# Optimization experiments

Hardware: AMD Instinct MI355X
Metric: run time of the kernel (lower is better)

The kernel has to match this reference:

```python
import jax, jax.numpy as jnp
import numpy as np

N_NODES = 50000
N_EDGES = 800000
N_ATOMS = 100
HID = 128
N_LAYERS = 3
OUT_LAYERS = 2
OUT_DIM = 1
N_GRAPHS = 1024
EPS = 1e-12  # F.normalize eps


def setup_inputs() -> dict:
    key = jax.random.key(0)
    ks = jax.random.split(key, 12)
    s = 0.05
    x_ori = jax.random.randint(ks[0], (N_NODES,), 0, N_ATOMS)
    edge_index = jax.random.randint(ks[1], (2, N_EDGES), 0, N_NODES)
    edge_attr = jax.random.normal(ks[2], (N_EDGES, 1), jnp.float32)
    batch_ids = jnp.sort(jax.random.randint(ks[3], (N_NODES,), 0, N_GRAPHS))
    embd_w = jax.random.normal(ks[4], (N_ATOMS, HID), jnp.float32) * s
    gamma_w = jnp.ones((N_LAYERS, N_ATOMS, 1), jnp.float32)  # reset_parameters sets ones
    w_atom_W = jax.random.normal(ks[5], (N_LAYERS, HID, HID), jnp.float32) * s
    w_atom_b = jax.random.normal(ks[6], (N_LAYERS, HID), jnp.float32) * s
    lin_W = jax.random.normal(ks[7], (OUT_LAYERS, HID, HID), jnp.float32) * s
    lin_b = jax.random.normal(ks[8], (OUT_LAYERS, HID), jnp.float32) * s
    wp_W = jax.random.normal(ks[9], (HID, OUT_DIM), jnp.float32) * s
    wp_b = jax.random.normal(ks[10], (OUT_DIM,), jnp.float32) * s
    return dict(x_ori=x_ori, edge_index=edge_index, edge_attr=edge_attr,
                batch_ids=batch_ids, embd_w=embd_w, gamma_w=gamma_w,
                w_atom_W=w_atom_W, w_atom_b=w_atom_b, lin_W=lin_W, lin_b=lin_b,
                wp_W=wp_W, wp_b=wp_b)


def reference(x_ori, edge_index, edge_attr, batch_ids, embd_w, gamma_w,
              w_atom_W, w_atom_b, lin_W, lin_b, wp_W, wp_b):
    src, dst = edge_index[0], edge_index[1]
    x = embd_w[x_ori]  # [N, H]
    for l in range(N_LAYERS):
        h = jax.nn.relu(x @ w_atom_W[l] + w_atom_b[l])            # [N, H]
        gam = jax.nn.sigmoid(gamma_w[l])[x_ori][dst]              # [E, 1]
        ew = jnp.exp(-gam * edge_attr ** 2)                       # [E, 1]
        msg = ew * h[src]                                         # [E, H] gather+weight
        agg = jax.ops.segment_sum(msg, dst, num_segments=N_NODES) # scatter-add
        y = agg + x
        nrm = jnp.maximum(jnp.linalg.norm(y, axis=1, keepdims=True), EPS)
        x = y / nrm                                               # F.normalize(., 2, 1)
    for i in range(OUT_LAYERS):
        x = jax.nn.relu(x @ lin_W[i] + lin_b[i])
    m_x = jax.ops.segment_sum(x, batch_ids, num_segments=N_GRAPHS)  # [G, H]
    props = m_x @ wp_W + wp_b                                      # [G, 1]
    return jnp.squeeze(props, axis=1)                              # [G]
```

## Files before the change

### kernel.cpp

```cpp
#include <hip/hip_runtime.h>
#include <hip/hip_bf16.h>
#include <math.h>

typedef __hip_bfloat16 bf16;
typedef unsigned int uint;
typedef unsigned short ushort;
typedef __attribute__((ext_vector_type(8))) short short8;
typedef __attribute__((ext_vector_type(4))) float f32x4;

#define HID 128
#define NN 50000
#define NE 800000
#define NG 1024
#define NA 100
#define CAP 64

__device__ __forceinline__ uint bf16_rne_hi(float f) {
    uint u = __float_as_uint(f);
    return (u + 0x7fffu + ((u >> 16) & 1u)) & 0xffff0000u;
}
__device__ __forceinline__ uint pack_bf16x2(float lo, float hi) {
    return (bf16_rne_hi(lo) >> 16) | bf16_rne_hi(hi);
}
__device__ __forceinline__ ushort bf16_rne(float f) {
    uint u = __float_as_uint(f);
    return (ushort)((u + 0x7fffu + ((u >> 16) & 1u)) >> 16);
}
__device__ __forceinline__ float load_f(const void* p, int i, int f32) {
    return f32 ? ((const float*)p)[i]
               : __uint_as_float((uint)((const ushort*)p)[i] << 16);
}
__device__ __forceinline__ int detect_f32(const void* emb) {
    const ushort* p = (const ushort*)emb;
    int lane = threadIdx.x & 63;
    float v = __uint_as_float((uint)p[lane * 4] << 16);
    int bad0 = (!(v == v) || fabsf(v) > 1e4f || (v != 0.0f && fabsf(v) < 1e-10f));
    float w = __uint_as_float((uint)p[lane * 4 + 2] << 16);
    int bad1 = (!(w == w) || fabsf(w) > 1e4f || (w != 0.0f && fabsf(w) < 1e-10f));
    int cnt = __popcll(__ballot(bad0)) + __popcll(__ballot(bad1));
    return cnt > 16;
}

#define EMB_BLKS   ((NN * 64) / 256)
#define PACKW_BLKS (5 * 16384 / 256)
#define CVT_CNT    (300 + 384 + 256 + 128 + 1)
#define CVT_BLKS   5
#define INITC_BLKS ((NN + 255) / 256)
#define PREP_B1    EMB_BLKS
#define PREP_B2    (PREP_B1 + PACKW_BLKS)
#define PREP_B3    (PREP_B2 + CVT_BLKS)
#define PREP_B4    (PREP_B3 + INITC_BLKS)
#define PREP_B5    (PREP_B4 + 4)
#define PREP_GRID  (PREP_B5 + 1)

__global__ void prep_k(const int* __restrict__ xo, const void* __restrict__ emb,
                       const void* __restrict__ gamw, const void* __restrict__ wAW,
                       const void* __restrict__ wAb, const void* __restrict__ linW,
                       const void* __restrict__ linb, const void* __restrict__ wpW,
                       const void* __restrict__ wpb,
                       uint* __restrict__ xb, ushort* __restrict__ Wp,
                       float* __restrict__ f_sgam, float* __restrict__ f_wAb,
                       float* __restrict__ f_linb, float* __restrict__ f_wp,
                       float* __restrict__ f_wpb, int* __restrict__ cursor,
                       float* __restrict__ grf, int* __restrict__ flag) {
    int f32 = detect_f32(emb);
    int b = blockIdx.x, t = threadIdx.x;
    if (b < PREP_B1) {
        int g = b * 256 + t;
        int node = g >> 6, c2 = g & 63;
        int base = xo[node] * HID + c2 * 2;
        xb[g] = pack_bf16x2(load_f(emb, base, f32), load_f(emb, base + 1, f32));
    } else if (b < PREP_B2) {
        int t2 = (b - PREP_B1) * 256 + t;
        int i   = t2 & 7;
        int n   = (t2 >> 3) & 15;
        int q   = (t2 >> 7) & 3;
        int j16 = (t2 >> 9) & 7;
        int ks  = (t2 >> 12) & 3;
        int mat = t2 >> 14;
        int k = ks * 32 + q * 8 + i;
        int j = j16 * 16 + n;
        const void* W = (mat < 3) ? wAW : linW;
        int off = ((mat < 3) ? mat : (mat - 3)) * 16384 + k * HID + j;
        Wp[t2] = bf16_rne(load_f(W, off, f32));
    } else if (b < PREP_B3) {
        int idx = (b - PREP_B2) * 256 + t;
        if (idx < 300) {
            float v = load_f(gamw, idx, f32);
            f_sgam[idx] = 1.0f / (1.0f + __expf(-v));
        } else if (idx < 684) {
            f_wAb[idx - 300] = load_f(wAb, idx - 300, f32);
        } else if (idx < 940) {
            f_linb[idx - 684] = load_f(linb, idx - 684, f32);
        } else if (idx < 1068) {
            f_wp[idx - 940] = load_f(wpW, idx - 940, f32);
        } else if (idx < CVT_CNT) {
            f_wpb[0] = load_f(wpb, 0, f32);
        }
    } else if (b < PREP_B4) {
        int n = (b - PREP_B3) * 256 + t;
        if (n < NN) cursor[n] = n * CAP;
    } else if (b < PREP_B5) {
        grf[(b - PREP_B4) * 256 + t] = 0.0f;
    } else {
        if (t == 0) *flag = f32;
    }
}

__device__ __forceinline__ void gemm_core(const uint* __restrict__ xb,
                                          const ushort* __restrict__ Wp,
                                          const float* __restrict__ bias,
                                          int m0, int lane,
                                          f32x4 acc0[8], f32x4 acc1[8]) {
    int ln15 = lane & 15;
    int q    = lane >> 4;
    int mA = min(m0 + ln15, NN - 1);
    int mB = min(m0 + 16 + ln15, NN - 1);
    const short8* A8 = (const short8*)xb;
    const short8* B8 = (const short8*)Wp;
#pragma unroll
    for (int j16 = 0; j16 < 8; ++j16) {
        float bv = bias[j16 * 16 + ln15];
        acc0[j16] = (f32x4){bv, bv, bv, bv};
        acc1[j16] = acc0[j16];
    }
#pragma unroll
    for (int ks = 0; ks < 4; ++ks) {
        short8 a0 = A8[mA * 16 + ks * 4 + q];
        short8 a1 = A8[mB * 16 + ks * 4 + q];
#pragma unroll
        for (int j16 = 0; j16 < 8; ++j16) {
            short8 b = B8[(ks * 8 + j16) * 64 + q * 16 + ln15];
            acc0[j16] = __builtin_amdgcn_mfma_f32_16x16x32_bf16(a0, b, acc0[j16], 0, 0, 0);
            acc1[j16] = __builtin_amdgcn_mfma_f32_16x16x32_bf16(a1, b, acc1[j16], 0, 0, 0);
        }
    }
}

__device__ __forceinline__ void gemm_store(f32x4 acc0[8], f32x4 acc1[8],
                                           int m0, int lane, uint* __restrict__ outb) {
    int ln15 = lane & 15;
    int q    = lane >> 4;
    ushort* ob = (ushort*)outb;
#pragma unroll
    for (int reg = 0; reg < 4; ++reg) {
        int n0 = m0 + q * 4 + reg;
        int n1 = n0 + 16;
#pragma unroll
        for (int j16 = 0; j16 < 8; ++j16) {
            if (n0 < NN)
                ob[(size_t)n0 * HID + j16 * 16 + ln15] = bf16_rne(fmaxf(acc0[j16][reg], 0.0f));
            if (n1 < NN)
                ob[(size_t)n1 * HID + j16 * 16 + ln15] = bf16_rne(fmaxf(acc1[j16][reg], 0.0f));
        }
    }
}

#define GEMM_BLKS ((NN + 127) / 128)
#define SCAT_BLKS (NE / 4 / 256)
__global__ __launch_bounds__(256) void work2_k(const uint* __restrict__ xb,
                                               const ushort* __restrict__ Wp,
                                               const float* __restrict__ bias,
                                               uint* __restrict__ outb,
                                               const int* __restrict__ esrc,
                                               const int* __restrict__ edst,
                                               const void* __restrict__ ea,
                                               const void* __restrict__ emb,
                                               int* __restrict__ cursor,
                                               uint* __restrict__ csr) {
    int b = blockIdx.x;
    if (b < GEMM_BLKS) {
        f32x4 acc0[8], acc1[8];
        int m0 = b * 128 + (threadIdx.x >> 6) * 32;
        gemm_core(xb, Wp, bias, m0, threadIdx.x & 63, acc0, acc1);
        gemm_store(acc0, acc1, m0, threadIdx.x & 63, outb);
    } else {
        int f32 = detect_f32(emb);
        int e0 = ((b - GEMM_BLKS) * 256 + threadIdx.x) * 4;
        int4 s4 = *(const int4*)(esrc + e0);
        int4 d4 = *(const int4*)(edst + e0);
        float a0, a1, a2, a3;
        if (f32) {
            float4 f = *(const float4*)((const float*)ea + e0);
            a0 = f.x; a1 = f.y; a2 = f.z; a3 = f.w;
        } else {
            ushort4 u = *(const ushort4*)((const ushort*)ea + e0);
            a0 = __uint_as_float((uint)u.x << 16);
            a1 = __uint_as_float((uint)u.y << 16);
            a2 = __uint_as_float((uint)u.z << 16);
            a3 = __uint_as_float((uint)u.w << 16);
        }
        int p0 = atomicAdd(&cursor[d4.x], 1);
        int p1 = atomicAdd(&cursor[d4.y], 1);
        int p2 = atomicAdd(&cursor[d4.z], 1);
        int p3 = atomicAdd(&cursor[d4.w], 1);
        if (p0 < d4.x * CAP + CAP) csr[p0] = (uint)(s4.x & 0xffff) | bf16_rne_hi(a0 * a0);
        if (p1 < d4.y * CAP + CAP) csr[p1] = (uint)(s4.y & 0xffff) | bf16_rne_hi(a1 * a1);
        if (p2 < d4.z * CAP + CAP) csr[p2] = (uint)(s4.z & 0xffff) | bf16_rne_hi(a2 * a2);
        if (p3 < d4.w * CAP + CAP) csr[p3] = (uint)(s4.w & 0xffff) | bf16_rne_hi(a3 * a3);
    }
}

__global__ __launch_bounds__(512) void gg_k(const int* __restrict__ cursor,
                                            const uint* __restrict__ csr,
                                            const int* __restrict__ xo,
                                            const float* __restrict__ sgam,
                                            const uint* __restrict__ hb_in,
                                            uint* __restrict__ xb,
                                            const ushort* __restrict__ Wp,
                                            const float* __restrict__ bias,
                                            uint* __restrict__ hb_out) {
    __shared__ uint lds_a[2048];
    int t = threadIdx.x;
    int w = t >> 6, lane = t & 63;
    int n0 = blockIdx.x * 32;

#pragma unroll
    for (int j4 = 0; j4 < 4; ++j4) {
        int j = w * 4 + j4;
        int n = n0 + j;
        if (n < NN) {
            int deg = min(cursor[n] - n * CAP, CAP);
            const uint* cp = csr + n * CAP;
            float g = sgam[xo[n]];
            float ax = 0.0f, ay = 0.0f;
            for (int e = 0; e < deg; e += 8) {
                uint4 c0 = *(const uint4*)(cp + e);
                uint4 c1 = *(const uint4*)(cp + e + 4);
                uint cc[8];
                cc[0] = c0.x; cc[1] = c0.y; cc[2] = c0.z; cc[3] = c0.w;
                cc[4] = c1.x; cc[5] = c1.y; cc[6] = c1.z; cc[7] = c1.w;
#pragma unroll
                for (int i = 1; i < 8; ++i) cc[i] = (e + i < deg) ? cc[i] : cc[0];
                uint v[8];
#pragma unroll
                for (int i = 0; i < 8; ++i) v[i] = hb_in[(cc[i] & 0xffffu) * 64 + lane];
                float we[8];
#pragma unroll
                for (int i = 0; i < 8; ++i) {
                    float x = __expf(-g * __uint_as_float(cc[i] & 0xffff0000u));
                    we[i] = (e + i < deg) ? x : 0.0f;
                }
#pragma unroll
                for (int i = 0; i < 8; ++i) {
                    ax = fmaf(we[i], __uint_as_float(v[i] << 16), ax);
                    ay = fmaf(we[i], __uint_as_float(v[i] & 0xffff0000u), ay);
                }
            }
            uint xv = xb[n * 64 + lane];
            float yx = ax + __uint_as_float(xv << 16);
            float yy = ay + __uint_as_float(xv & 0xffff0000u);
            float ss = yx * yx + yy * yy;
#pragma unroll
            for (int m = 32; m; m >>= 1) ss += __shfl_xor(ss, m);
            float inv = 1.0f / fmaxf(sqrtf(ss), 1e-12f);
            uint o = pack_bf16x2(yx * inv, yy * inv);
            xb[n * 64 + lane] = o;
            int rt = j >> 4, m = j & 15;
            int ks = lane >> 4, q = (lane >> 2) & 3;
            lds_a[(((rt * 4 + ks) * 64) + q * 16 + m) * 4 + (lane & 3)] = o;
        }
    }
    __syncthreads();

    int ln15 = lane & 15, q = lane >> 4;
    const short8* A8 = (const short8*)lds_a;
    const short8* B8 = (const short8*)Wp;
    f32x4 acc[2];
    {
        float bv = bias[w * 16 + ln15];
        acc[0] = (f32x4){bv, bv, bv, bv};
        acc[1] = acc[0];
    }
#pragma unroll
    for (int ks = 0; ks < 4; ++ks) {
        short8 b = B8[(ks * 8 + w) * 64 + q * 16 + ln15];
#pragma unroll
        for (int rt = 0; rt < 2; ++rt) {
            short8 a = A8[(rt * 4 + ks) * 64 + lane];
            acc[rt] = __builtin_amdgcn_mfma_f32_16x16x32_bf16(a, b, acc[rt], 0, 0, 0);
        }
    }
    ushort* ob = (ushort*)hb_out;
#pragma unroll
    for (int rt = 0; rt < 2; ++rt) {
#pragma unroll
        for (int reg = 0; reg < 4; ++reg) {
            int n = n0 + rt * 16 + q * 4 + reg;
            if (n < NN)
                ob[(size_t)n * HID + w * 16 + ln15] = bf16_rne(fmaxf(acc[rt][reg], 0.0f));
        }
    }
}

__global__ __launch_bounds__(256) void gemm5_graph_k(const uint* __restrict__ xb,
                                                     const ushort* __restrict__ Wp,
                                                     const float* __restrict__ bias,
                                                     const float* __restrict__ wp,
                                                     const int* __restrict__ batch,
                                                     float* __restrict__ grf) {
    int lane = threadIdx.x & 63;
    int ln15 = lane & 15;
    int q    = lane >> 4;
    int m0 = blockIdx.x * 128 + (threadIdx.x >> 6) * 32;
    f32x4 acc0[8], acc1[8];
    gemm_core(xb, Wp, bias, m0, lane, acc0, acc1);
    float wpv[8];
#pragma unroll
    for (int j16 = 0; j16 < 8; ++j16) wpv[j16] = wp[j16 * 16 + ln15];
#pragma unroll
    for (int half = 0; half < 2; ++half) {
#pragma unroll
        for (int reg = 0; reg < 4; ++reg) {
            float s = 0.0f;
#pragma unroll
            for (int j16 = 0; j16 < 8; ++j16) {
                float v = half ? acc1[j16][reg] : acc0[j16][reg];
                s = fmaf(fmaxf(v, 0.0f), wpv[j16], s);
            }
#pragma unroll
            for (int m = 1; m < 16; m <<= 1) s += __shfl_xor(s, m);
            int n = m0 + half * 16 + q * 4 + reg;
            if (ln15 == 0 && n < NN) atomicAdd(&grf[batch[n]], s);
        }
    }
}

__global__ void out_k(const float* __restrict__ grf, const float* __restrict__ wpb,
                      void* __restrict__ out, const int* __restrict__ flag) {
    int g = blockIdx.x * 256 + threadIdx.x;
    if (g >= NG) return;
    float r = grf[g] + wpb[0];
    if (*flag) ((float*)out)[g] = r;
    else       ((bf16*)out)[g] = __float2bfloat16(r);
}

extern "C" void kernel_launch(void* const* d_in, const int* in_sizes, int n_in,
                              void* d_out, int out_size, void* d_ws, size_t ws_size,
                              hipStream_t stream) {
    const int*  xo    = (const int*)d_in[0];
    const int*  ei    = (const int*)d_in[1];
    const int*  src   = ei;
    const int*  dst   = ei + NE;
    const void* ea    = d_in[2];
    const int*  batch = (const int*)d_in[3];
    const void* emb   = d_in[4];
    const void* gamw  = d_in[5];
    const void* wAW   = d_in[6];
    const void* wAb   = d_in[7];
    const void* linW  = d_in[8];
    const void* linb  = d_in[9];
    const void* wpW   = d_in[10];
    const void* wpb   = d_in[11];

    uint*  xb     = (uint*)d_ws;
    uint*  hA     = xb + (size_t)NN * 64;
    uint*  hB     = hA + (size_t)NN * 64;
    uint*  csr    = hB + (size_t)NN * 64;
    int*   cursor = (int*)(csr + (size_t)NN * CAP);
    float* grf    = (float*)(cursor + NN);
    float* P      = grf + NG;
    float* f_sgam = P;
    float* f_wAb  = f_sgam + 304;
    float* f_linb = f_wAb + 384;
    float* f_wp   = f_linb + 256;
    float* f_wpb  = f_wp + 128;
    int*   flag   = (int*)(f_wpb + 8);
    ushort* Wp    = (ushort*)(flag + 8);

    prep_k<<<PREP_GRID, 256, 0, stream>>>(xo, emb, gamw, wAW, wAb, linW, linb, wpW, wpb,
                                          xb, Wp, f_sgam, f_wAb, f_linb, f_wp, f_wpb,
                                          cursor, grf, flag);

    work2_k<<<GEMM_BLKS + SCAT_BLKS, 256, 0, stream>>>(xb, Wp, f_wAb, hA,
                                                       src, dst, ea, emb, cursor, csr);

    const int GG_GRID = (NN + 31) / 32;
    gg_k<<<GG_GRID, 512, 0, stream>>>(cursor, csr, xo, f_sgam,       hA, xb,
                                      Wp + 1 * 16384, f_wAb + 128, hB);
    gg_k<<<GG_GRID, 512, 0, stream>>>(cursor, csr, xo, f_sgam + 100, hB, xb,
                                      Wp + 2 * 16384, f_wAb + 256, hA);
    gg_k<<<GG_GRID, 512, 0, stream>>>(cursor, csr, xo, f_sgam + 200, hA, xb,
                                      Wp + 3 * 16384, f_linb,       hB);

    gemm5_graph_k<<<GEMM_BLKS, 256, 0, stream>>>(hB, Wp + 4 * 16384, f_linb + HID,
                                                 f_wp, batch, grf);
    out_k<<<(NG + 255) / 256, 256, 0, stream>>>(grf, f_wpb, d_out, flag);
}
```

Baseline: 296.5 us.

## Fuse final MLP layer and graph pooling into last gather layer; restructure prep

```diff
diff --git a/kernel.cpp b/kernel.cpp
--- a/kernel.cpp
+++ b/kernel.cpp
@@ -41,142 +41,33 @@
     return cnt > 16;
 }
 
+#define SCAT_BLKS  (NE / 4 / 256)
 #define EMB_BLKS   ((NN * 64) / 256)
 #define PACKW_BLKS (5 * 16384 / 256)
 #define CVT_CNT    (300 + 384 + 256 + 128 + 1)
 #define CVT_BLKS   5
-#define INITC_BLKS ((NN + 255) / 256)
-#define PREP_B1    EMB_BLKS
-#define PREP_B2    (PREP_B1 + PACKW_BLKS)
-#define PREP_B3    (PREP_B2 + CVT_BLKS)
-#define PREP_B4    (PREP_B3 + INITC_BLKS)
-#define PREP_B5    (PREP_B4 + 4)
-#define PREP_GRID  (PREP_B5 + 1)
-
-__global__ void prep_k(const int* __restrict__ xo, const void* __restrict__ emb,
-                       const void* __restrict__ gamw, const void* __restrict__ wAW,
-                       const void* __restrict__ wAb, const void* __restrict__ linW,
-                       const void* __restrict__ linb, const void* __restrict__ wpW,
-                       const void* __restrict__ wpb,
-                       uint* __restrict__ xb, ushort* __restrict__ Wp,
-                       float* __restrict__ f_sgam, float* __restrict__ f_wAb,
-                       float* __restrict__ f_linb, float* __restrict__ f_wp,
-                       float* __restrict__ f_wpb, int* __restrict__ cursor,
-                       float* __restrict__ grf, int* __restrict__ flag) {
+#define W1_B1      SCAT_BLKS
+#define W1_B2      (W1_B1 + EMB_BLKS)
+#define W1_B3      (W1_B2 + PACKW_BLKS)
+#define W1_B4      (W1_B3 + CVT_BLKS)
+#define W1_GRID    (W1_B4 + 1)
+
+__global__ void work1_k(const int* __restrict__ xo, const void* __restrict__ emb,
+                        const void* __restrict__ gamw, const void* __restrict__ wAW,
+                        const void* __restrict__ wAb, const void* __restrict__ linW,
+                        const void* __restrict__ linb, const void* __restrict__ wpW,
+                        const void* __restrict__ wpb,
+                        const int* __restrict__ esrc, const int* __restrict__ edst,
+                        const void* __restrict__ ea,
+                        uint* __restrict__ xb, ushort* __restrict__ Wp,
+                        float* __restrict__ f_sgam, float* __restrict__ f_wAb,
+                        float* __restrict__ f_linb, float* __restrict__ f_wp,
+                        float* __restrict__ f_wpb, int* __restrict__ cursor,
+                        uint* __restrict__ csr, int* __restrict__ flag) {
     int f32 = detect_f32(emb);
     int b = blockIdx.x, t = threadIdx.x;
-    if (b < PREP_B1) {
-        int g = b * 256 + t;
-        int node = g >> 6, c2 = g & 63;
-        int base = xo[node] * HID + c2 * 2;
-        xb[g] = pack_bf16x2(load_f(emb, base, f32), load_f(emb, base + 1, f32));
-    } else if (b < PREP_B2) {
-        int t2 = (b - PREP_B1) * 256 + t;
-        int i   = t2 & 7;
-        int n   = (t2 >> 3) & 15;
-        int q   = (t2 >> 7) & 3;
-        int j16 = (t2 >> 9) & 7;
-        int ks  = (t2 >> 12) & 3;
-        int mat = t2 >> 14;
-        int k = ks * 32 + q * 8 + i;
-        int j = j16 * 16 + n;
-        const void* W = (mat < 3) ? wAW : linW;
-        int off = ((mat < 3) ? mat : (mat - 3)) * 16384 + k * HID + j;
-        Wp[t2] = bf16_rne(load_f(W, off, f32));
-    } else if (b < PREP_B3) {
-        int idx = (b - PREP_B2) * 256 + t;
-        if (idx < 300) {
-            float v = load_f(gamw, idx, f32);
-            f_sgam[idx] = 1.0f / (1.0f + __expf(-v));
-        } else if (idx < 684) {
-            f_wAb[idx - 300] = load_f(wAb, idx - 300, f32);
-        } else if (idx < 940) {
-            f_linb[idx - 684] = load_f(linb, idx - 684, f32);
-        } else if (idx < 1068) {
-            f_wp[idx - 940] = load_f(wpW, idx - 940, f32);
-        } else if (idx < CVT_CNT) {
-            f_wpb[0] = load_f(wpb, 0, f32);
-        }
-    } else if (b < PREP_B4) {
-        int n = (b - PREP_B3) * 256 + t;
-        if (n < NN) cursor[n] = n * CAP;
-    } else if (b < PREP_B5) {
-        grf[(b - PREP_B4) * 256 + t] = 0.0f;
-    } else {
-        if (t == 0) *flag = f32;
-    }
-}
-
-__device__ __forceinline__ void gemm_core(const uint* __restrict__ xb,
-                                          const ushort* __restrict__ Wp,
-                                          const float* __restrict__ bias,
-                                          int m0, int lane,
-                                          f32x4 acc0[8], f32x4 acc1[8]) {
-    int ln15 = lane & 15;
-    int q    = lane >> 4;
-    int mA = min(m0 + ln15, NN - 1);
-    int mB = min(m0 + 16 + ln15, NN - 1);
-    const short8* A8 = (const short8*)xb;
-    const short8* B8 = (const short8*)Wp;
-#pragma unroll
-    for (int j16 = 0; j16 < 8; ++j16) {
-        float bv = bias[j16 * 16 + ln15];
-        acc0[j16] = (f32x4){bv, bv, bv, bv};
-        acc1[j16] = acc0[j16];
-    }
-#pragma unroll
-    for (int ks = 0; ks < 4; ++ks) {
-        short8 a0 = A8[mA * 16 + ks * 4 + q];
-        short8 a1 = A8[mB * 16 + ks * 4 + q];
-#pragma unroll
-        for (int j16 = 0; j16 < 8; ++j16) {
-            short8 b = B8[(ks * 8 + j16) * 64 + q * 16 + ln15];
-            acc0[j16] = __builtin_amdgcn_mfma_f32_16x16x32_bf16(a0, b, acc0[j16], 0, 0, 0);
-            acc1[j16] = __builtin_amdgcn_mfma_f32_16x16x32_bf16(a1, b, acc1[j16], 0, 0, 0);
-        }
-    }
-}
-
-__device__ __forceinline__ void gemm_store(f32x4 acc0[8], f32x4 acc1[8],
-                                           int m0, int lane, uint* __restrict__ outb) {
-    int ln15 = lane & 15;
-    int q    = lane >> 4;
-    ushort* ob = (ushort*)outb;
-#pragma unroll
-    for (int reg = 0; reg < 4; ++reg) {
-        int n0 = m0 + q * 4 + reg;
-        int n1 = n0 + 16;
-#pragma unroll
-        for (int j16 = 0; j16 < 8; ++j16) {
-            if (n0 < NN)
-                ob[(size_t)n0 * HID + j16 * 16 + ln15] = bf16_rne(fmaxf(acc0[j16][reg], 0.0f));
-            if (n1 < NN)
-                ob[(size_t)n1 * HID + j16 * 16 + ln15] = bf16_rne(fmaxf(acc1[j16][reg], 0.0f));
-        }
-    }
-}
-
-#define GEMM_BLKS ((NN + 127) / 128)
-#define SCAT_BLKS (NE / 4 / 256)
-__global__ __launch_bounds__(256) void work2_k(const uint* __restrict__ xb,
-                                               const ushort* __restrict__ Wp,
-                                               const float* __restrict__ bias,
-                                               uint* __restrict__ outb,
-                                               const int* __restrict__ esrc,
-                                               const int* __restrict__ edst,
-                                               const void* __restrict__ ea,
-                                               const void* __restrict__ emb,
-                                               int* __restrict__ cursor,
-                                               uint* __restrict__ csr) {
-    int b = blockIdx.x;
-    if (b < GEMM_BLKS) {
-        f32x4 acc0[8], acc1[8];
-        int m0 = b * 128 + (threadIdx.x >> 6) * 32;
-        gemm_core(xb, Wp, bias, m0, threadIdx.x & 63, acc0, acc1);
-        gemm_store(acc0, acc1, m0, threadIdx.x & 63, outb);
-    } else {
-        int f32 = detect_f32(emb);
-        int e0 = ((b - GEMM_BLKS) * 256 + threadIdx.x) * 4;
+    if (b < W1_B1) {
+        int e0 = (b * 256 + t) * 4;
         int4 s4 = *(const int4*)(esrc + e0);
         int4 d4 = *(const int4*)(edst + e0);
         float a0, a1, a2, a3;
@@ -194,13 +85,103 @@
         int p1 = atomicAdd(&cursor[d4.y], 1);
         int p2 = atomicAdd(&cursor[d4.z], 1);
         int p3 = atomicAdd(&cursor[d4.w], 1);
-        if (p0 < d4.x * CAP + CAP) csr[p0] = (uint)(s4.x & 0xffff) | bf16_rne_hi(a0 * a0);
-        if (p1 < d4.y * CAP + CAP) csr[p1] = (uint)(s4.y & 0xffff) | bf16_rne_hi(a1 * a1);
-        if (p2 < d4.z * CAP + CAP) csr[p2] = (uint)(s4.z & 0xffff) | bf16_rne_hi(a2 * a2);
-        if (p3 < d4.w * CAP + CAP) csr[p3] = (uint)(s4.w & 0xffff) | bf16_rne_hi(a3 * a3);
-    }
-}
-
+        if (p0 < CAP) csr[d4.x * CAP + p0] = (uint)(s4.x & 0xffff) | bf16_rne_hi(a0 * a0);
+        if (p1 < CAP) csr[d4.y * CAP + p1] = (uint)(s4.y & 0xffff) | bf16_rne_hi(a1 * a1);
+        if (p2 < CAP) csr[d4.z * CAP + p2] = (uint)(s4.z & 0xffff) | bf16_rne_hi(a2 * a2);
+        if (p3 < CAP) csr[d4.w * CAP + p3] = (uint)(s4.w & 0xffff) | bf16_rne_hi(a3 * a3);
+    } else if (b < W1_B2) {
+        int g = (b - W1_B1) * 256 + t;
+        int node = g >> 6, c2 = g & 63;
+        int base = xo[node] * HID + c2 * 2;
+        xb[g] = pack_bf16x2(load_f(emb, base, f32), load_f(emb, base + 1, f32));
+    } else if (b < W1_B3) {
+        int t2 = (b - W1_B2) * 256 + t;
+        int i   = t2 & 7;
+        int n   = (t2 >> 3) & 15;
+        int q   = (t2 >> 7) & 3;
+        int j16 = (t2 >> 9) & 7;
+        int ks  = (t2 >> 12) & 3;
+        int mat = t2 >> 14;
+        int k = ks * 32 + q * 8 + i;
+        int j = j16 * 16 + n;
+        const void* W = (mat < 3) ? wAW : linW;
+        int off = ((mat < 3) ? mat : (mat - 3)) * 16384 + k * HID + j;
+        Wp[t2] = bf16_rne(load_f(W, off, f32));
+    } else if (b < W1_B4) {
+        int idx = (b - W1_B3) * 256 + t;
+        if (idx < 300) {
+            float v = load_f(gamw, idx, f32);
+            f_sgam[idx] = 1.0f / (1.0f + __expf(-v));
+        } else if (idx < 684) {
+            f_wAb[idx - 300] = load_f(wAb, idx - 300, f32);
+        } else if (idx < 940) {
+            f_linb[idx - 684] = load_f(linb, idx - 684, f32);
+        } else if (idx < 1068) {
+            f_wp[idx - 940] = load_f(wpW, idx - 940, f32);
+        } else if (idx < CVT_CNT) {
+            f_wpb[0] = load_f(wpb, 0, f32);
+        }
+    } else {
+        if (t == 0) *flag = f32;
+    }
+}
+
+__device__ __forceinline__ void gemm_core(const uint* __restrict__ xb,
+                                          const ushort* __restrict__ Wp,
+                                          const float* __restrict__ bias,
+                                          int m0, int lane,
+                                          f32x4 acc0[8], f32x4 acc1[8]) {
+    int ln15 = lane & 15;
+    int q    = lane >> 4;
+    int mA = min(m0 + ln15, NN - 1);
+    int mB = min(m0 + 16 + ln15, NN - 1);
+    const short8* A8 = (const short8*)xb;
+    const short8* B8 = (const short8*)Wp;
+#pragma unroll
+    for (int j16 = 0; j16 < 8; ++j16) {
+        float bv = bias[j16 * 16 + ln15];
+        acc0[j16] = (f32x4){bv, bv, bv, bv};
+        acc1[j16] = acc0[j16];
+    }
+#pragma unroll
+    for (int ks = 0; ks < 4; ++ks) {
+        short8 a0 = A8[mA * 16 + ks * 4 + q];
+        short8 a1 = A8[mB * 16 + ks * 4 + q];
+#pragma unroll
+        for (int j16 = 0; j16 < 8; ++j16) {
+            short8 b = B8[(ks * 8 + j16) * 64 + q * 16 + ln15];
+            acc0[j16] = __builtin_amdgcn_mfma_f32_16x16x32_bf16(a0, b, acc0[j16], 0, 0, 0);
+            acc1[j16] = __builtin_amdgcn_mfma_f32_16x16x32_bf16(a1, b, acc1[j16], 0, 0, 0);
+        }
+    }
+}
+
+#define GEMM_BLKS ((NN + 127) / 128)
+__global__ __launch_bounds__(256) void gemm_mfma_k(const uint* __restrict__ xb,
+                                                   const ushort* __restrict__ Wp,
+                                                   const float* __restrict__ bias,
+                                                   uint* __restrict__ outb) {
+    int lane = threadIdx.x & 63;
+    int ln15 = lane & 15, q = lane >> 4;
+    int m0 = blockIdx.x * 128 + (threadIdx.x >> 6) * 32;
+    f32x4 acc0[8], acc1[8];
+    gemm_core(xb, Wp, bias, m0, lane, acc0, acc1);
+    ushort* ob = (ushort*)outb;
+#pragma unroll
+    for (int reg = 0; reg < 4; ++reg) {
+        int n0 = m0 + q * 4 + reg;
+        int n1 = n0 + 16;
+#pragma unroll
+        for (int j16 = 0; j16 < 8; ++j16) {
+            if (n0 < NN)
+                ob[(size_t)n0 * HID + j16 * 16 + ln15] = bf16_rne(fmaxf(acc0[j16][reg], 0.0f));
+            if (n1 < NN)
+                ob[(size_t)n1 * HID + j16 * 16 + ln15] = bf16_rne(fmaxf(acc1[j16][reg], 0.0f));
+        }
+    }
+}
+
+template <int LAST>
 __global__ __launch_bounds__(512) void gg_k(const int* __restrict__ cursor,
                                             const uint* __restrict__ csr,
                                             const int* __restrict__ xo,
@@ -209,8 +190,15 @@
                                             uint* __restrict__ xb,
                                             const ushort* __restrict__ Wp,
                                             const float* __restrict__ bias,
-                                            uint* __restrict__ hb_out) {
+                                            uint* __restrict__ hb_out,
+                                            const ushort* __restrict__ Wp2,
+                                            const float* __restrict__ bias2,
+                                            const float* __restrict__ wp,
+                                            const int* __restrict__ batch,
+                                            float* __restrict__ grf) {
     __shared__ uint lds_a[2048];
+    __shared__ ushort lds_h[LAST ? 16384 / 2 : 2];
+    __shared__ float lds_g[LAST ? 32 : 1];
     int t = threadIdx.x;
     int w = t >> 6, lane = t & 63;
     int n0 = blockIdx.x * 32;
@@ -220,7 +208,7 @@
         int j = w * 4 + j4;
         int n = n0 + j;
         if (n < NN) {
-            int deg = min(cursor[n] - n * CAP, CAP);
+            int deg = min(cursor[n], CAP);
             const uint* cp = csr + n * CAP;
             float g = sgam[xo[n]];
             float ax = 0.0f, ay = 0.0f;
@@ -255,12 +243,13 @@
             for (int m = 32; m; m >>= 1) ss += __shfl_xor(ss, m);
             float inv = 1.0f / fmaxf(sqrtf(ss), 1e-12f);
             uint o = pack_bf16x2(yx * inv, yy * inv);
-            xb[n * 64 + lane] = o;
+            if (!LAST) xb[n * 64 + lane] = o;
             int rt = j >> 4, m = j & 15;
             int ks = lane >> 4, q = (lane >> 2) & 3;
             lds_a[(((rt * 4 + ks) * 64) + q * 16 + m) * 4 + (lane & 3)] = o;
         }
     }
+    if (LAST && t < 32) lds_g[t] = 0.0f;
     __syncthreads();
 
     int ln15 = lane & 15, q = lane >> 4;
@@ -281,48 +270,67 @@
             acc[rt] = __builtin_amdgcn_mfma_f32_16x16x32_bf16(a, b, acc[rt], 0, 0, 0);
         }
     }
-    ushort* ob = (ushort*)hb_out;
+    if (!LAST) {
+        ushort* ob = (ushort*)hb_out;
+#pragma unroll
+        for (int rt = 0; rt < 2; ++rt) {
+#pragma unroll
+            for (int reg = 0; reg < 4; ++reg) {
+                int n = n0 + rt * 16 + q * 4 + reg;
+                if (n < NN)
+                    ob[(size_t)n * HID + w * 16 + ln15] = bf16_rne(fmaxf(acc[rt][reg], 0.0f));
+            }
+        }
+        return;
+    }
+
+    {
+        int c = w * 16 + ln15;
+        int ks2 = c >> 5, q2 = (c >> 3) & 3, i2 = c & 7;
+#pragma unroll
+        for (int rt = 0; rt < 2; ++rt) {
+#pragma unroll
+            for (int reg = 0; reg < 4; ++reg) {
+                int m2 = q * 4 + reg;
+                lds_h[(((rt * 4 + ks2) * 64) + q2 * 16 + m2) * 8 + i2] =
+                    bf16_rne(fmaxf(acc[rt][reg], 0.0f));
+            }
+        }
+    }
+    __syncthreads();
+    const short8* H8 = (const short8*)lds_h;
+    const short8* B8b = (const short8*)Wp2;
+    f32x4 acc2[2];
+    {
+        float bv = bias2[w * 16 + ln15];
+        acc2[0] = (f32x4){bv, bv, bv, bv};
+        acc2[1] = acc2[0];
+    }
+#pragma unroll
+    for (int ks = 0; ks < 4; ++ks) {
+        short8 b = B8b[(ks * 8 + w) * 64 + q * 16 + ln15];
+#pragma unroll
+        for (int rt = 0; rt < 2; ++rt) {
+            short8 a = H8[(rt * 4 + ks) * 64 + lane];
+            acc2[rt] = __builtin_amdgcn_mfma_f32_16x16x32_bf16(a, b, acc2[rt], 0, 0, 0);
+        }
+    }
+    float wpc = wp[w * 16 + ln15];
 #pragma unroll
     for (int rt = 0; rt < 2; ++rt) {
 #pragma unroll
         for (int reg = 0; reg < 4; ++reg) {
-            int n = n0 + rt * 16 + q * 4 + reg;
-            if (n < NN)
-                ob[(size_t)n * HID + w * 16 + ln15] = bf16_rne(fmaxf(acc[rt][reg], 0.0f));
-        }
-    }
-}
-
-__global__ __launch_bounds__(256) void gemm5_graph_k(const uint* __restrict__ xb,
-                                                     const ushort* __restrict__ Wp,
-                                                     const float* __restrict__ bias,
-                                                     const float* __restrict__ wp,
-                                                     const int* __restrict__ batch,
-                                                     float* __restrict__ grf) {
-    int lane = threadIdx.x & 63;
-    int ln15 = lane & 15;
-    int q    = lane >> 4;
-    int m0 = blockIdx.x * 128 + (threadIdx.x >> 6) * 32;
-    f32x4 acc0[8], acc1[8];
-    gemm_core(xb, Wp, bias, m0, lane, acc0, acc1);
-    float wpv[8];
-#pragma unroll
-    for (int j16 = 0; j16 < 8; ++j16) wpv[j16] = wp[j16 * 16 + ln15];
-#pragma unroll
-    for (int half = 0; half < 2; ++half) {
-#pragma unroll
-        for (int reg = 0; reg < 4; ++reg) {
-            float s = 0.0f;
-#pragma unroll
-            for (int j16 = 0; j16 < 8; ++j16) {
-                float v = half ? acc1[j16][reg] : acc0[j16][reg];
-                s = fmaf(fmaxf(v, 0.0f), wpv[j16], s);
-            }
+            float s = fmaxf(acc2[rt][reg], 0.0f) * wpc;
 #pragma unroll
             for (int m = 1; m < 16; m <<= 1) s += __shfl_xor(s, m);
-            int n = m0 + half * 16 + q * 4 + reg;
-            if (ln15 == 0 && n < NN) atomicAdd(&grf[batch[n]], s);
-        }
+            int r = rt * 16 + q * 4 + reg;
+            if (ln15 == 0 && n0 + r < NN) atomicAdd(&lds_g[r], s);
+        }
+    }
+    __syncthreads();
+    if (t < 32) {
+        int n = n0 + t;
+        if (n < NN) atomicAdd(&grf[batch[n]], lds_g[t]);
     }
 }
 
@@ -368,22 +376,25 @@
     int*   flag   = (int*)(f_wpb + 8);
     ushort* Wp    = (ushort*)(flag + 8);
 
-    prep_k<<<PREP_GRID, 256, 0, stream>>>(xo, emb, gamw, wAW, wAb, linW, linb, wpW, wpb,
-                                          xb, Wp, f_sgam, f_wAb, f_linb, f_wp, f_wpb,
-                                          cursor, grf, flag);
-
-    work2_k<<<GEMM_BLKS + SCAT_BLKS, 256, 0, stream>>>(xb, Wp, f_wAb, hA,
-                                                       src, dst, ea, emb, cursor, csr);
+    hipMemsetAsync(cursor, 0, (NN + NG) * sizeof(int), stream);
+
+    work1_k<<<W1_GRID, 256, 0, stream>>>(xo, emb, gamw, wAW, wAb, linW, linb, wpW, wpb,
+                                         src, dst, ea,
+                                         xb, Wp, f_sgam, f_wAb, f_linb, f_wp, f_wpb,
+                                         cursor, csr, flag);
+
+    gemm_mfma_k<<<GEMM_BLKS, 256, 0, stream>>>(xb, Wp, f_wAb, hA);
 
     const int GG_GRID = (NN + 31) / 32;
-    gg_k<<<GG_GRID, 512, 0, stream>>>(cursor, csr, xo, f_sgam,       hA, xb,
-                                      Wp + 1 * 16384, f_wAb + 128, hB);
-    gg_k<<<GG_GRID, 512, 0, stream>>>(cursor, csr, xo, f_sgam + 100, hB, xb,
-                                      Wp + 2 * 16384, f_wAb + 256, hA);
-    gg_k<<<GG_GRID, 512, 0, stream>>>(cursor, csr, xo, f_sgam + 200, hA, xb,
-                                      Wp + 3 * 16384, f_linb,       hB);
-
-    gemm5_graph_k<<<GEMM_BLKS, 256, 0, stream>>>(hB, Wp + 4 * 16384, f_linb + HID,
-                                                 f_wp, batch, grf);
+    gg_k<0><<<GG_GRID, 512, 0, stream>>>(cursor, csr, xo, f_sgam,       hA, xb,
+                                         Wp + 1 * 16384, f_wAb + 128, hB,
+                                         Wp, f_wAb, f_wp, batch, grf);
+    gg_k<0><<<GG_GRID, 512, 0, stream>>>(cursor, csr, xo, f_sgam + 100, hB, xb,
+                                         Wp + 2 * 16384, f_wAb + 256, hA,
+                                         Wp, f_wAb, f_wp, batch, grf);
+    gg_k<1><<<GG_GRID, 512, 0, stream>>>(cursor, csr, xo, f_sgam + 200, hA, xb,
+                                         Wp + 3 * 16384, f_linb,       hB,
+                                         Wp + 4 * 16384, f_linb + 128, f_wp, batch, grf);
+
     out_k<<<(NG + 255) / 256, 256, 0, stream>>>(grf, f_wpb, d_out, flag);
 }
```

After: 333.8 us. +12.6%, slower.

## Move edge CSR scatter into prep kernel and split layer-0 GEMM out

Applied to the files above, without the earlier changes.

```diff
diff --git a/kernel.cpp b/kernel.cpp
--- a/kernel.cpp
+++ b/kernel.cpp
@@ -41,142 +41,33 @@
     return cnt > 16;
 }
 
+#define SCAT_BLKS  (NE / 4 / 256)
 #define EMB_BLKS   ((NN * 64) / 256)
 #define PACKW_BLKS (5 * 16384 / 256)
 #define CVT_CNT    (300 + 384 + 256 + 128 + 1)
 #define CVT_BLKS   5
-#define INITC_BLKS ((NN + 255) / 256)
-#define PREP_B1    EMB_BLKS
-#define PREP_B2    (PREP_B1 + PACKW_BLKS)
-#define PREP_B3    (PREP_B2 + CVT_BLKS)
-#define PREP_B4    (PREP_B3 + INITC_BLKS)
-#define PREP_B5    (PREP_B4 + 4)
-#define PREP_GRID  (PREP_B5 + 1)
-
-__global__ void prep_k(const int* __restrict__ xo, const void* __restrict__ emb,
-                       const void* __restrict__ gamw, const void* __restrict__ wAW,
-                       const void* __restrict__ wAb, const void* __restrict__ linW,
-                       const void* __restrict__ linb, const void* __restrict__ wpW,
-                       const void* __restrict__ wpb,
-                       uint* __restrict__ xb, ushort* __restrict__ Wp,
-                       float* __restrict__ f_sgam, float* __restrict__ f_wAb,
-                       float* __restrict__ f_linb, float* __restrict__ f_wp,
-                       float* __restrict__ f_wpb, int* __restrict__ cursor,
-                       float* __restrict__ grf, int* __restrict__ flag) {
+#define W1_B1      SCAT_BLKS
+#define W1_B2      (W1_B1 + EMB_BLKS)
+#define W1_B3      (W1_B2 + PACKW_BLKS)
+#define W1_B4      (W1_B3 + CVT_BLKS)
+#define W1_GRID    (W1_B4 + 1)
+
+__global__ void work1_k(const int* __restrict__ xo, const void* __restrict__ emb,
+                        const void* __restrict__ gamw, const void* __restrict__ wAW,
+                        const void* __restrict__ wAb, const void* __restrict__ linW,
+                        const void* __restrict__ linb, const void* __restrict__ wpW,
+                        const void* __restrict__ wpb,
+                        const int* __restrict__ esrc, const int* __restrict__ edst,
+                        const void* __restrict__ ea,
+                        uint* __restrict__ xb, ushort* __restrict__ Wp,
+                        float* __restrict__ f_sgam, float* __restrict__ f_wAb,
+                        float* __restrict__ f_linb, float* __restrict__ f_wp,
+                        float* __restrict__ f_wpb, int* __restrict__ cursor,
+                        uint* __restrict__ csr, int* __restrict__ flag) {
     int f32 = detect_f32(emb);
     int b = blockIdx.x, t = threadIdx.x;
-    if (b < PREP_B1) {
-        int g = b * 256 + t;
-        int node = g >> 6, c2 = g & 63;
-        int base = xo[node] * HID + c2 * 2;
-        xb[g] = pack_bf16x2(load_f(emb, base, f32), load_f(emb, base + 1, f32));
-    } else if (b < PREP_B2) {
-        int t2 = (b - PREP_B1) * 256 + t;
-        int i   = t2 & 7;
-        int n   = (t2 >> 3) & 15;
-        int q   = (t2 >> 7) & 3;
-        int j16 = (t2 >> 9) & 7;
-        int ks  = (t2 >> 12) & 3;
-        int mat = t2 >> 14;
-        int k = ks * 32 + q * 8 + i;
-        int j = j16 * 16 + n;
-        const void* W = (mat < 3) ? wAW : linW;
-        int off = ((mat < 3) ? mat : (mat - 3)) * 16384 + k * HID + j;
-        Wp[t2] = bf16_rne(load_f(W, off, f32));
-    } else if (b < PREP_B3) {
-        int idx = (b - PREP_B2) * 256 + t;
-        if (idx < 300) {
-            float v = load_f(gamw, idx, f32);
-            f_sgam[idx] = 1.0f / (1.0f + __expf(-v));
-        } else if (idx < 684) {
-            f_wAb[idx - 300] = load_f(wAb, idx - 300, f32);
-        } else if (idx < 940) {
-            f_linb[idx - 684] = load_f(linb, idx - 684, f32);
-        } else if (idx < 1068) {
-            f_wp[idx - 940] = load_f(wpW, idx - 940, f32);
-        } else if (idx < CVT_CNT) {
-            f_wpb[0] = load_f(wpb, 0, f32);
-        }
-    } else if (b < PREP_B4) {
-        int n = (b - PREP_B3) * 256 + t;
-        if (n < NN) cursor[n] = n * CAP;
-    } else if (b < PREP_B5) {
-        grf[(b - PREP_B4) * 256 + t] = 0.0f;
-    } else {
-        if (t == 0) *flag = f32;
-    }
-}
-
-__device__ __forceinline__ void gemm_core(const uint* __restrict__ xb,
-                                          const ushort* __restrict__ Wp,
-                                          const float* __restrict__ bias,
-                                          int m0, int lane,
-                                          f32x4 acc0[8], f32x4 acc1[8]) {
-    int ln15 = lane & 15;
-    int q    = lane >> 4;
-    int mA = min(m0 + ln15, NN - 1);
-    int mB = min(m0 + 16 + ln15, NN - 1);
-    const short8* A8 = (const short8*)xb;
-    const short8* B8 = (const short8*)Wp;
-#pragma unroll
-    for (int j16 = 0; j16 < 8; ++j16) {
-        float bv = bias[j16 * 16 + ln15];
-        acc0[j16] = (f32x4){bv, bv, bv, bv};
-        acc1[j16] = acc0[j16];
-    }
-#pragma unroll
-    for (int ks = 0; ks < 4; ++ks) {
-        short8 a0 = A8[mA * 16 + ks * 4 + q];
-        short8 a1 = A8[mB * 16 + ks * 4 + q];
-#pragma unroll
-        for (int j16 = 0; j16 < 8; ++j16) {
-            short8 b = B8[(ks * 8 + j16) * 64 + q * 16 + ln15];
-            acc0[j16] = __builtin_amdgcn_mfma_f32_16x16x32_bf16(a0, b, acc0[j16], 0, 0, 0);
-            acc1[j16] = __builtin_amdgcn_mfma_f32_16x16x32_bf16(a1, b, acc1[j16], 0, 0, 0);
-        }
-    }
-}
-
-__device__ __forceinline__ void gemm_store(f32x4 acc0[8], f32x4 acc1[8],
-                                           int m0, int lane, uint* __restrict__ outb) {
-    int ln15 = lane & 15;
-    int q    = lane >> 4;
-    ushort* ob = (ushort*)outb;
-#pragma unroll
-    for (int reg = 0; reg < 4; ++reg) {
-        int n0 = m0 + q * 4 + reg;
-        int n1 = n0 + 16;
-#pragma unroll
-        for (int j16 = 0; j16 < 8; ++j16) {
-            if (n0 < NN)
-                ob[(size_t)n0 * HID + j16 * 16 + ln15] = bf16_rne(fmaxf(acc0[j16][reg], 0.0f));
-            if (n1 < NN)
-                ob[(size_t)n1 * HID + j16 * 16 + ln15] = bf16_rne(fmaxf(acc1[j16][reg], 0.0f));
-        }
-    }
-}
-
-#define GEMM_BLKS ((NN + 127) / 128)
-#define SCAT_BLKS (NE / 4 / 256)
-__global__ __launch_bounds__(256) void work2_k(const uint* __restrict__ xb,
-                                               const ushort* __restrict__ Wp,
-                                               const float* __restrict__ bias,
-                                               uint* __restrict__ outb,
-                                               const int* __restrict__ esrc,
-                                               const int* __restrict__ edst,
-                                               const void* __restrict__ ea,
-                                               const void* __restrict__ emb,
-                                               int* __restrict__ cursor,
-                                               uint* __restrict__ csr) {
-    int b = blockIdx.x;
-    if (b < GEMM_BLKS) {
-        f32x4 acc0[8], acc1[8];
-        int m0 = b * 128 + (threadIdx.x >> 6) * 32;
-        gemm_core(xb, Wp, bias, m0, threadIdx.x & 63, acc0, acc1);
-        gemm_store(acc0, acc1, m0, threadIdx.x & 63, outb);
-    } else {
-        int f32 = detect_f32(emb);
-        int e0 = ((b - GEMM_BLKS) * 256 + threadIdx.x) * 4;
+    if (b < W1_B1) {
+        int e0 = (b * 256 + t) * 4;
         int4 s4 = *(const int4*)(esrc + e0);
         int4 d4 = *(const int4*)(edst + e0);
         float a0, a1, a2, a3;
@@ -194,10 +85,99 @@
         int p1 = atomicAdd(&cursor[d4.y], 1);
         int p2 = atomicAdd(&cursor[d4.z], 1);
         int p3 = atomicAdd(&cursor[d4.w], 1);
-        if (p0 < d4.x * CAP + CAP) csr[p0] = (uint)(s4.x & 0xffff) | bf16_rne_hi(a0 * a0);
-        if (p1 < d4.y * CAP + CAP) csr[p1] = (uint)(s4.y & 0xffff) | bf16_rne_hi(a1 * a1);
-        if (p2 < d4.z * CAP + CAP) csr[p2] = (uint)(s4.z & 0xffff) | bf16_rne_hi(a2 * a2);
-        if (p3 < d4.w * CAP + CAP) csr[p3] = (uint)(s4.w & 0xffff) | bf16_rne_hi(a3 * a3);
+        if (p0 < CAP) csr[d4.x * CAP + p0] = (uint)(s4.x & 0xffff) | bf16_rne_hi(a0 * a0);
+        if (p1 < CAP) csr[d4.y * CAP + p1] = (uint)(s4.y & 0xffff) | bf16_rne_hi(a1 * a1);
+        if (p2 < CAP) csr[d4.z * CAP + p2] = (uint)(s4.z & 0xffff) | bf16_rne_hi(a2 * a2);
+        if (p3 < CAP) csr[d4.w * CAP + p3] = (uint)(s4.w & 0xffff) | bf16_rne_hi(a3 * a3);
+    } else if (b < W1_B2) {
+        int g = (b - W1_B1) * 256 + t;
+        int node = g >> 6, c2 = g & 63;
+        int base = xo[node] * HID + c2 * 2;
+        xb[g] = pack_bf16x2(load_f(emb, base, f32), load_f(emb, base + 1, f32));
+    } else if (b < W1_B3) {
+        int t2 = (b - W1_B2) * 256 + t;
+        int i   = t2 & 7;
+        int n   = (t2 >> 3) & 15;
+        int q   = (t2 >> 7) & 3;
+        int j16 = (t2 >> 9) & 7;
+        int ks  = (t2 >> 12) & 3;
+        int mat = t2 >> 14;
+        int k = ks * 32 + q * 8 + i;
+        int j = j16 * 16 + n;
+        const void* W = (mat < 3) ? wAW : linW;
+        int off = ((mat < 3) ? mat : (mat - 3)) * 16384 + k * HID + j;
+        Wp[t2] = bf16_rne(load_f(W, off, f32));
+    } else if (b < W1_B4) {
+        int idx = (b - W1_B3) * 256 + t;
+        if (idx < 300) {
+            float v = load_f(gamw, idx, f32);
+            f_sgam[idx] = 1.0f / (1.0f + __expf(-v));
+        } else if (idx < 684) {
+            f_wAb[idx - 300] = load_f(wAb, idx - 300, f32);
+        } else if (idx < 940) {
+            f_linb[idx - 684] = load_f(linb, idx - 684, f32);
+        } else if (idx < 1068) {
+            f_wp[idx - 940] = load_f(wpW, idx - 940, f32);
+        } else if (idx < CVT_CNT) {
+            f_wpb[0] = load_f(wpb, 0, f32);
+        }
+    } else {
+        if (t == 0) *flag = f32;
+    }
+}
+
+__device__ __forceinline__ void gemm_core(const uint* __restrict__ xb,
+                                          const ushort* __restrict__ Wp,
+                                          const float* __restrict__ bias,
+                                          int m0, int lane,
+                                          f32x4 acc0[8], f32x4 acc1[8]) {
+    int ln15 = lane & 15;
+    int q    = lane >> 4;
+    int mA = min(m0 + ln15, NN - 1);
+    int mB = min(m0 + 16 + ln15, NN - 1);
+    const short8* A8 = (const short8*)xb;
+    const short8* B8 = (const short8*)Wp;
+#pragma unroll
+    for (int j16 = 0; j16 < 8; ++j16) {
+        float bv = bias[j16 * 16 + ln15];
+        acc0[j16] = (f32x4){bv, bv, bv, bv};
+        acc1[j16] = acc0[j16];
+    }
+#pragma unroll
+    for (int ks = 0; ks < 4; ++ks) {
+        short8 a0 = A8[mA * 16 + ks * 4 + q];
+        short8 a1 = A8[mB * 16 + ks * 4 + q];
+#pragma unroll
+        for (int j16 = 0; j16 < 8; ++j16) {
+            short8 b = B8[(ks * 8 + j16) * 64 + q * 16 + ln15];
+            acc0[j16] = __builtin_amdgcn_mfma_f32_16x16x32_bf16(a0, b, acc0[j16], 0, 0, 0);
+            acc1[j16] = __builtin_amdgcn_mfma_f32_16x16x32_bf16(a1, b, acc1[j16], 0, 0, 0);
+        }
+    }
+}
+
+#define GEMM_BLKS ((NN + 127) / 128)
+__global__ __launch_bounds__(256) void gemm_mfma_k(const uint* __restrict__ xb,
+                                                   const ushort* __restrict__ Wp,
+                                                   const float* __restrict__ bias,
+                                                   uint* __restrict__ outb) {
+    int lane = threadIdx.x & 63;
+    int ln15 = lane & 15, q = lane >> 4;
+    int m0 = blockIdx.x * 128 + (threadIdx.x >> 6) * 32;
+    f32x4 acc0[8], acc1[8];
+    gemm_core(xb, Wp, bias, m0, lane, acc0, acc1);
+    ushort* ob = (ushort*)outb;
+#pragma unroll
+    for (int reg = 0; reg < 4; ++reg) {
+        int n0 = m0 + q * 4 + reg;
+        int n1 = n0 + 16;
+#pragma unroll
+        for (int j16 = 0; j16 < 8; ++j16) {
+            if (n0 < NN)
+                ob[(size_t)n0 * HID + j16 * 16 + ln15] = bf16_rne(fmaxf(acc0[j16][reg], 0.0f));
+            if (n1 < NN)
+                ob[(size_t)n1 * HID + j16 * 16 + ln15] = bf16_rne(fmaxf(acc1[j16][reg], 0.0f));
+        }
     }
 }
 
@@ -220,7 +200,7 @@
         int j = w * 4 + j4;
         int n = n0 + j;
         if (n < NN) {
-            int deg = min(cursor[n] - n * CAP, CAP);
+            int deg = min(cursor[n], CAP);
             const uint* cp = csr + n * CAP;
             float g = sgam[xo[n]];
             float ax = 0.0f, ay = 0.0f;
@@ -368,12 +348,14 @@
     int*   flag   = (int*)(f_wpb + 8);
     ushort* Wp    = (ushort*)(flag + 8);
 
-    prep_k<<<PREP_GRID, 256, 0, stream>>>(xo, emb, gamw, wAW, wAb, linW, linb, wpW, wpb,
-                                          xb, Wp, f_sgam, f_wAb, f_linb, f_wp, f_wpb,
-                                          cursor, grf, flag);
-
-    work2_k<<<GEMM_BLKS + SCAT_BLKS, 256, 0, stream>>>(xb, Wp, f_wAb, hA,
-                                                       src, dst, ea, emb, cursor, csr);
+    hipMemsetAsync(cursor, 0, (NN + NG) * sizeof(int), stream);
+
+    work1_k<<<W1_GRID, 256, 0, stream>>>(xo, emb, gamw, wAW, wAb, linW, linb, wpW, wpb,
+                                         src, dst, ea,
+                                         xb, Wp, f_sgam, f_wAb, f_linb, f_wp, f_wpb,
+                                         cursor, csr, flag);
+
+    gemm_mfma_k<<<GEMM_BLKS, 256, 0, stream>>>(xb, Wp, f_wAb, hA);
 
     const int GG_GRID = (NN + 31) / 32;
     gg_k<<<GG_GRID, 512, 0, stream>>>(cursor, csr, xo, f_sgam,       hA, xb,
```

New measurement: 299.7 us. Within noise of the previous version (+1.1%).
